# Optimization experiments

Measured on AMD Instinct MI355X. Metric: run time of the kernel, lower is better.

The kernel has to match this reference:

```python
import jax, jax.numpy as jnp
import numpy as np

N_WORDS = 30000
EMB_DIM = 784          # must be a perfect square
MAT_DIM = 28           # sqrt(784)
BATCH = 256
SEQ_LEN = 64


def setup_inputs() -> dict:
    key = jax.random.key(0)
    k_sent, k_w = jax.random.split(key)
    # token ids in [1, N_WORDS]; row 0 of the table is the identity (neutral) element
    sent = jax.random.randint(k_sent, (BATCH, SEQ_LEN), 1, N_WORDS + 1, dtype=jnp.int64) \
        if jax.config.jax_enable_x64 else \
        jax.random.randint(k_sent, (BATCH, SEQ_LEN), 1, N_WORDS + 1, dtype=jnp.int32)
    # 'identity' initialization: N(0, 0.1) + flattened identity, prepended identity neutral row
    eye_flat = jnp.eye(MAT_DIM, dtype=jnp.float32).reshape(-1)        # [784]
    init_w = 0.1 * jax.random.normal(k_w, (N_WORDS, EMB_DIM), dtype=jnp.float32) + eye_flat
    lookup_weight = jnp.concatenate([eye_flat[None, :], init_w], axis=0)  # [N_WORDS+1, 784]
    return {"sent": sent, "lookup_weight": lookup_weight}


def reference(sent, lookup_weight):
    # CMOW: embedding lookup, reshape each word vector to a 28x28 matrix,
    # then a left-to-right chain of matrix products over the sequence.
    B, S = sent.shape
    mats = lookup_weight[sent].reshape(B, S, MAT_DIM, MAT_DIM)   # [B, S, 28, 28]
    # Log-depth parallel prefix product over the sequence axis (matmul is associative).
    prods = jax.lax.associative_scan(lambda a, b: a @ b, mats, axis=1)
    cur_emb = prods[:, -1]                                       # [B, 28, 28]
    return cur_emb.reshape(-1, EMB_DIM)                          # [B, 784]
```

## Files before the change

kernel.cpp:

```cpp
#include <hip/hip_runtime.h>
#include <hip/hip_bf16.h>


namespace {
constexpr int MD   = 28;
constexpr int EMB  = 784;
constexpr int SEQ  = 64;
constexpr int BATCH = 256;
}

__global__ __launch_bounds__(256, 1)
void w2m_chain_kernel(const int* __restrict__ sent,
                      const float* __restrict__ W,
                      float* __restrict__ out) {
  __shared__ __align__(16) float R[EMB];
  __shared__ __align__(16) float Mb[2][EMB];

  const int b   = blockIdx.x;
  const int tid = threadIdx.x;
  const bool act = tid < 196;
  const int i  = tid / 14;
  const int j  = tid % 14;
  const int r0 = 2 * i;
  const int c0 = 2 * j;
  const int* srow = sent + b * SEQ;

  float4 pre0, pre1;
  if (act) {
    ((float4*)R)[tid] = ((const float4*)(W + (size_t)srow[0] * EMB))[tid];
    pre0 = ((const float4*)(W + (size_t)srow[1] * EMB))[tid];
    pre1 = ((const float4*)(W + (size_t)srow[2] * EMB))[tid];
  }

  float a00 = 0.f, a01 = 0.f, a10 = 0.f, a11 = 0.f;

  for (int t = 1; t < SEQ; ++t) {
    float* __restrict__ M = Mb[t & 1];
    if (act) ((float4*)M)[tid] = pre0;
    pre0 = pre1;
    if (t + 2 < SEQ) {
      if (act) pre1 = ((const float4*)(W + (size_t)srow[t + 2] * EMB))[tid];
    }
    __syncthreads();

    a00 = a01 = a10 = a11 = 0.f;
    if (act) {
      const float* __restrict__ Ra = R + r0 * MD;
      const float* __restrict__ Rb = Ra + MD;
      const float* __restrict__ Mc = M + c0;
#pragma unroll
      for (int k = 0; k < MD; ++k) {
        const float ra = Ra[k];
        const float rb = Rb[k];
        const float m0 = Mc[k * MD];
        const float m1 = Mc[k * MD + 1];
        a00 = fmaf(ra, m0, a00);
        a01 = fmaf(ra, m1, a01);
        a10 = fmaf(rb, m0, a10);
        a11 = fmaf(rb, m1, a11);
      }
    }
    __syncthreads();

    if (act && t < SEQ - 1) {
      R[r0 * MD + c0]          = a00;
      R[r0 * MD + c0 + 1]      = a01;
      R[(r0 + 1) * MD + c0]     = a10;
      R[(r0 + 1) * MD + c0 + 1] = a11;
    }
  }

  if (act) {
    float* __restrict__ o = out + (size_t)b * EMB;
    o[r0 * MD + c0]           = a00;
    o[r0 * MD + c0 + 1]       = a01;
    o[(r0 + 1) * MD + c0]     = a10;
    o[(r0 + 1) * MD + c0 + 1] = a11;
  }
}

extern "C" void kernel_launch(void* const* d_in, const int* in_sizes, int n_in,
                              void* d_out, int out_size, void* d_ws, size_t ws_size,
                              hipStream_t stream) {
  const int*   sent = (const int*)d_in[0];
  const float* W    = (const float*)d_in[1];
  float*       out  = (float*)d_out;
  (void)in_sizes; (void)n_in; (void)out_size; (void)d_ws; (void)ws_size;

  w2m_chain_kernel<<<BATCH, 256, 0, stream>>>(sent, W, out);
}
```

Before: 159.7 us.

## Split sequence chain into parallel segments with tree-reduction combine kernel

```diff
diff --git a/kernel.cpp b/kernel.cpp
--- a/kernel.cpp
+++ b/kernel.cpp
@@ -2,80 +2,162 @@
 #include <hip/hip_bf16.h>
 
 
+typedef float f32x4 __attribute__((ext_vector_type(4)));
+
 namespace {
-constexpr int MD   = 28;
-constexpr int EMB  = 784;
-constexpr int SEQ  = 64;
+constexpr int MD  = 28;
+constexpr int EMB = 784;
+constexpr int SEQ = 64;
 constexpr int BATCH = 256;
+constexpr int SEG = 8;
+constexpr int LEN = 8;
+}
+
+__device__ __forceinline__ void kloop(const float* __restrict__ A,
+                                      const float* __restrict__ B,
+                                      int r0, int c0,
+                                      f32x4& a0, f32x4& a1, f32x4& a2, f32x4& a3) {
+  f32x4 z = {0.f, 0.f, 0.f, 0.f};
+  a0 = a1 = a2 = a3 = z;
+#pragma unroll
+  for (int k = 0; k < MD; ++k) {
+    f32x4 rv = *reinterpret_cast<const f32x4*>(A + k * MD + r0);
+    f32x4 mv = *reinterpret_cast<const f32x4*>(B + k * MD + c0);
+    a0 += rv[0] * mv;
+    a1 += rv[1] * mv;
+    a2 += rv[2] * mv;
+    a3 += rv[3] * mv;
+  }
+}
+
+__device__ __forceinline__ void store_T(float* __restrict__ D, int r0, int c0,
+                                        const f32x4& a0, const f32x4& a1,
+                                        const f32x4& a2, const f32x4& a3) {
+#pragma unroll
+  for (int cc = 0; cc < 4; ++cc) {
+    f32x4 v = { a0[cc], a1[cc], a2[cc], a3[cc] };
+    *reinterpret_cast<f32x4*>(D + (c0 + cc) * MD + r0) = v;
+  }
+}
+
+__device__ __forceinline__ void store_N(float* __restrict__ D, int r0, int c0,
+                                        const f32x4& a0, const f32x4& a1,
+                                        const f32x4& a2, const f32x4& a3) {
+  *reinterpret_cast<f32x4*>(D + (r0 + 0) * MD + c0) = a0;
+  *reinterpret_cast<f32x4*>(D + (r0 + 1) * MD + c0) = a1;
+  *reinterpret_cast<f32x4*>(D + (r0 + 2) * MD + c0) = a2;
+  *reinterpret_cast<f32x4*>(D + (r0 + 3) * MD + c0) = a3;
+}
+
+__global__ __launch_bounds__(64, 1)
+void w2m_partial(const int* __restrict__ sent,
+                 const float* __restrict__ W,
+                 float* __restrict__ ws) {
+  __shared__ __align__(16) float Ms[2][EMB];
+  __shared__ __align__(16) float Rt[2][EMB];
+
+  const int blk   = blockIdx.x;
+  const int batch = blk >> 3;
+  const int seg   = blk & 7;
+  const int lane  = threadIdx.x;
+  const bool act  = lane < 49;
+  const int i = lane / 7, j = lane % 7;
+  const int r0 = 4 * i, c0 = 4 * j;
+  const int* srow = sent + batch * SEQ + seg * LEN;
+
+  f32x4 sA0, sA1, sA2, sA3;
+  f32x4 sB0, sB1, sB2, sB3;
+
+  auto gload = [&](int t, f32x4& v0, f32x4& v1, f32x4& v2, f32x4& v3) {
+    const f32x4* src = reinterpret_cast<const f32x4*>(W + (size_t)srow[t] * EMB);
+    v0 = src[lane];
+    v1 = src[64 + lane];
+    v2 = src[128 + lane];
+    if (lane < 4) v3 = src[192 + lane];
+  };
+  auto lwrite = [&](float* dst, const f32x4& v0, const f32x4& v1,
+                    const f32x4& v2, const f32x4& v3) {
+    f32x4* d = reinterpret_cast<f32x4*>(dst);
+    d[lane] = v0;
+    d[64 + lane] = v1;
+    d[128 + lane] = v2;
+    if (lane < 4) d[192 + lane] = v3;
+  };
+
+  gload(0, sA0, sA1, sA2, sA3);
+  if (act) {
+#pragma unroll
+    for (int cc = 0; cc < 4; ++cc) {
+      int d = (c0 + cc) - r0;
+      f32x4 v = { d == 0 ? 1.f : 0.f, d == 1 ? 1.f : 0.f,
+                  d == 2 ? 1.f : 0.f, d == 3 ? 1.f : 0.f };
+      *reinterpret_cast<f32x4*>(&Rt[0][(c0 + cc) * MD + r0]) = v;
+    }
+  }
+  lwrite(Ms[0], sA0, sA1, sA2, sA3);
+  gload(1, sB0, sB1, sB2, sB3);
+
+  f32x4 a0, a1, a2, a3;
+#pragma unroll 1
+  for (int tp = 0; tp < LEN; tp += 2) {
+    lwrite(Ms[1], sB0, sB1, sB2, sB3);
+    if (tp + 2 < LEN) gload(tp + 2, sA0, sA1, sA2, sA3);
+    if (act) {
+      kloop(Rt[0], Ms[0], r0, c0, a0, a1, a2, a3);
+      store_T(Rt[1], r0, c0, a0, a1, a2, a3);
+    }
+    if (tp + 2 < LEN) lwrite(Ms[0], sA0, sA1, sA2, sA3);
+    if (tp + 3 < LEN) gload(tp + 3, sB0, sB1, sB2, sB3);
+    if (act) {
+      kloop(Rt[1], Ms[1], r0, c0, a0, a1, a2, a3);
+      if (tp + 1 < LEN - 1) {
+        store_T(Rt[0], r0, c0, a0, a1, a2, a3);
+      } else {
+        float* pb = ws + (size_t)(batch * SEG + seg) * EMB;
+        if (seg & 1) store_N(pb, r0, c0, a0, a1, a2, a3);
+        else         store_T(pb, r0, c0, a0, a1, a2, a3);
+      }
+    }
+  }
 }
 
 __global__ __launch_bounds__(256, 1)
-void w2m_chain_kernel(const int* __restrict__ sent,
-                      const float* __restrict__ W,
-                      float* __restrict__ out) {
-  __shared__ __align__(16) float R[EMB];
-  __shared__ __align__(16) float Mb[2][EMB];
+void w2m_combine(const float* __restrict__ ws, float* __restrict__ out) {
+  __shared__ __align__(16) float P[SEG][EMB];
+  __shared__ __align__(16) float Q[4][EMB];
+  __shared__ __align__(16) float Rl[2][EMB];
 
-  const int b   = blockIdx.x;
-  const int tid = threadIdx.x;
-  const bool act = tid < 196;
-  const int i  = tid / 14;
-  const int j  = tid % 14;
-  const int r0 = 2 * i;
-  const int c0 = 2 * j;
-  const int* srow = sent + b * SEQ;
+  const int batch = blockIdx.x;
+  const int tid   = threadIdx.x;
+  const int w     = tid >> 6;
+  const int lane  = tid & 63;
+  const bool act  = lane < 49;
+  const int i = lane / 7, j = lane % 7;
+  const int r0 = 4 * i, c0 = 4 * j;
 
-  float4 pre0, pre1;
+  {
+    const f32x4* src = reinterpret_cast<const f32x4*>(ws + (size_t)batch * SEG * EMB);
+    f32x4* dst = reinterpret_cast<f32x4*>(&P[0][0]);
+    for (int u = tid; u < SEG * EMB / 4; u += 256) dst[u] = src[u];
+  }
+  __syncthreads();
+
+  f32x4 a0, a1, a2, a3;
   if (act) {
-    ((float4*)R)[tid] = ((const float4*)(W + (size_t)srow[0] * EMB))[tid];
-    pre0 = ((const float4*)(W + (size_t)srow[1] * EMB))[tid];
-    pre1 = ((const float4*)(W + (size_t)srow[2] * EMB))[tid];
+    kloop(P[2 * w], P[2 * w + 1], r0, c0, a0, a1, a2, a3);
+    if (w & 1) store_N(Q[w], r0, c0, a0, a1, a2, a3);
+    else       store_T(Q[w], r0, c0, a0, a1, a2, a3);
   }
-
-  float a00 = 0.f, a01 = 0.f, a10 = 0.f, a11 = 0.f;
-
-  for (int t = 1; t < SEQ; ++t) {
-    float* __restrict__ M = Mb[t & 1];
-    if (act) ((float4*)M)[tid] = pre0;
-    pre0 = pre1;
-    if (t + 2 < SEQ) {
-      if (act) pre1 = ((const float4*)(W + (size_t)srow[t + 2] * EMB))[tid];
-    }
-    __syncthreads();
-
-    a00 = a01 = a10 = a11 = 0.f;
-    if (act) {
-      const float* __restrict__ Ra = R + r0 * MD;
-      const float* __restrict__ Rb = Ra + MD;
-      const float* __restrict__ Mc = M + c0;
-#pragma unroll
-      for (int k = 0; k < MD; ++k) {
-        const float ra = Ra[k];
-        const float rb = Rb[k];
-        const float m0 = Mc[k * MD];
-        const float m1 = Mc[k * MD + 1];
-        a00 = fmaf(ra, m0, a00);
-        a01 = fmaf(ra, m1, a01);
-        a10 = fmaf(rb, m0, a10);
-        a11 = fmaf(rb, m1, a11);
-      }
-    }
-    __syncthreads();
-
-    if (act && t < SEQ - 1) {
-      R[r0 * MD + c0]          = a00;
-      R[r0 * MD + c0 + 1]      = a01;
-      R[(r0 + 1) * MD + c0]     = a10;
-      R[(r0 + 1) * MD + c0 + 1] = a11;
-    }
+  __syncthreads();
+  if (w < 2 && act) {
+    kloop(Q[2 * w], Q[2 * w + 1], r0, c0, a0, a1, a2, a3);
+    if (w & 1) store_N(Rl[w], r0, c0, a0, a1, a2, a3);
+    else       store_T(Rl[w], r0, c0, a0, a1, a2, a3);
   }
-
-  if (act) {
-    float* __restrict__ o = out + (size_t)b * EMB;
-    o[r0 * MD + c0]           = a00;
-    o[r0 * MD + c0 + 1]       = a01;
-    o[(r0 + 1) * MD + c0]     = a10;
-    o[(r0 + 1) * MD + c0 + 1] = a11;
+  __syncthreads();
+  if (w == 0 && act) {
+    kloop(Rl[0], Rl[1], r0, c0, a0, a1, a2, a3);
+    store_N(out + (size_t)batch * EMB, r0, c0, a0, a1, a2, a3);
   }
 }
 
@@ -85,7 +167,9 @@
   const int*   sent = (const int*)d_in[0];
   const float* W    = (const float*)d_in[1];
   float*       out  = (float*)d_out;
-  (void)in_sizes; (void)n_in; (void)out_size; (void)d_ws; (void)ws_size;
+  float*       ws   = (float*)d_ws;
+  (void)in_sizes; (void)n_in; (void)out_size; (void)ws_size;
 
-  w2m_chain_kernel<<<BATCH, 256, 0, stream>>>(sent, W, out);
+  w2m_partial<<<BATCH * SEG, 64, 0, stream>>>(sent, W, ws);
+  w2m_combine<<<BATCH, 256, 0, stream>>>(ws, out);
 }
```

New measurement: 141.5 us. 1.13x faster.
